# Optimization experiments

Measured on AMD Instinct MI355X. Metric: run time of the kernel, lower is better.

## Reference

```python
import jax, jax.numpy as jnp
import numpy as np
from jax import lax

N_GROUPS = 128
EPS = 1e-5


def _instance_norm(x):
    # x: [B, C, H, W]; per-sample per-channel normalization over spatial dims
    mean = jnp.mean(x, axis=(2, 3), keepdims=True)
    var = jnp.mean(jnp.square(x - mean), axis=(2, 3), keepdims=True)
    return (x - mean) * lax.rsqrt(var + EPS)


def _reflect_pad(x, p):
    return jnp.pad(x, ((0, 0), (0, 0), (p, p), (p, p)), mode='reflect')


def _conv(x, w, groups):
    # x: [N, Cin, H, W], w: [Cout, Cin/groups, kh, kw], VALID padding
    return lax.conv_general_dilated(
        x, w, window_strides=(1, 1), padding='VALID',
        dimension_numbers=('NCHW', 'OIHW', 'NCHW'),
        feature_group_count=groups)


def _forward_single(xi, ws, wp, b):
    # xi: [1, C, H, W]; ws: [C_mid, C/G, k, k]; wp: [C_pw, C_mid/G, 1, 1]; b: [C_pw]
    k = ws.shape[-1]
    p = (k - 1) // 2  # k=3 -> ceil/floor both 1
    y = _conv(_reflect_pad(xi, p), ws, N_GROUPS)
    y = _conv(y, wp, N_GROUPS) + b[None, :, None, None]
    return y


def setup_inputs() -> dict:
    key = jax.random.key(0)
    ks = jax.random.split(key, 6)
    B, C, H, W = 4, 512, 128, 128
    x = jax.random.normal(ks[0], (B, C, H, W), dtype=jnp.float32)
    w_spatial = jax.random.normal(ks[1], (B, 512, 4, 3, 3), dtype=jnp.float32) * 0.05
    w_pointwise = jax.random.normal(ks[2], (B, 128, 4, 1, 1), dtype=jnp.float32) * 0.05
    bias = jax.random.normal(ks[3], (B, 128), dtype=jnp.float32) * 0.05
    conv_w = jax.random.normal(ks[4], (512, 512, 3, 3), dtype=jnp.float32) * 0.02
    conv_b = jax.random.normal(ks[5], (512,), dtype=jnp.float32) * 0.02
    return {"x": x, "w_spatial": w_spatial, "w_pointwise": w_pointwise,
            "bias": bias, "conv_w": conv_w, "conv_b": conv_b}


def reference(x, w_spatial, w_pointwise, bias, conv_w, conv_b):
    B, C, H, W = x.shape
    x = _instance_norm(x)
    # per-sample grouped spatial + pointwise conv, vmapped over batch
    ys = jax.vmap(_forward_single)(x[:, None], w_spatial, w_pointwise, bias)
    # ys: [B, 1, C_pw, H, W] -> concat along channel dim as in torch.cat(dim=1)
    ys = ys.reshape(1, B * ys.shape[2], H, W)
    # final standard conv, reflect padding (1,1), kernel 3
    out = _conv(_reflect_pad(ys, 1), conv_w, 1) + conv_b[None, :, None, None]
    return out
```

## Files before the change

kernel.cpp:

```cpp
#include <hip/hip_runtime.h>
#include <hip/hip_bf16.h>


typedef unsigned short u16;
typedef __attribute__((ext_vector_type(8))) short bf16x8;
typedef __attribute__((ext_vector_type(4))) float f32x4;

#define HW 16384
#define NBC 2048

__device__ __forceinline__ int refl(int i) {
    return i < 0 ? -i : (i > 127 ? 254 - i : i);
}

__device__ __forceinline__ u16 f2bf(float f) {
    union { float f; unsigned u; } x; x.f = f;
    unsigned r = x.u + 0x7fffu + ((x.u >> 16) & 1u);
    return (u16)(r >> 16);
}

__device__ __forceinline__ void load_lds16(const u16* g, u16* l) {
    __builtin_amdgcn_global_load_lds(
        (const __attribute__((address_space(1))) unsigned int*)g,
        (__attribute__((address_space(3))) unsigned int*)l, 16, 0, 0);
}

__device__ __forceinline__ void load_lds4(const float* g, float* l) {
    __builtin_amdgcn_global_load_lds(
        (const __attribute__((address_space(1))) unsigned int*)g,
        (__attribute__((address_space(3))) unsigned int*)l, 4, 0, 0);
}

__global__ __launch_bounds__(256) void stats_kernel(
        const float* __restrict__ x, float* __restrict__ mean,
        float* __restrict__ rstd) {
    int bc = blockIdx.x;
    const float4* p4 = (const float4*)(x + (size_t)bc * HW);
    float s = 0.f, ss = 0.f;
    for (int i = threadIdx.x; i < HW / 4; i += 256) {
        float4 v = p4[i];
        s  += v.x + v.y + v.z + v.w;
        ss += v.x * v.x + v.y * v.y + v.z * v.z + v.w * v.w;
    }
    for (int o = 32; o >= 1; o >>= 1) {
        s  += __shfl_down(s, o);
        ss += __shfl_down(ss, o);
    }
    __shared__ float sm[4], sm2[4];
    int wid = threadIdx.x >> 6, lane = threadIdx.x & 63;
    if (lane == 0) { sm[wid] = s; sm2[wid] = ss; }
    __syncthreads();
    if (threadIdx.x == 0) {
        float S = sm[0] + sm[1] + sm[2] + sm[3];
        float SS = sm2[0] + sm2[1] + sm2[2] + sm2[3];
        float m = S * (1.f / HW);
        float var = SS * (1.f / HW) - m * m;
        mean[bc] = m;
        rstd[bc] = rsqrtf(var + 1e-5f);
    }
}

__global__ __launch_bounds__(256) void weff_kernel(
        const float* __restrict__ wsp, const float* __restrict__ wpw,
        float* __restrict__ we) {
    int idx = blockIdx.x * 256 + threadIdx.x;
    if (idx >= 4 * 128 * 4 * 9) return;
    int k = idx % 9;
    int c = (idx / 9) & 3;
    int g = (idx / 36) & 127;
    int b = idx / 4608;
    float acc = 0.f;
#pragma unroll
    for (int m = 0; m < 4; ++m) {
        acc += wpw[(b * 128 + g) * 4 + m] *
               wsp[(((size_t)b * 512 + g * 4 + m) * 4 + c) * 9 + k];
    }
    we[idx] = acc;
}

__global__ __launch_bounds__(256) void wpack_kernel(
        const float* __restrict__ cw, u16* __restrict__ wT) {
    __shared__ float s[512 * 10];
    int t = threadIdx.x, co = blockIdx.x;
    const float* src = cw + (size_t)co * 4608;
    for (int i = t; i < 4608; i += 256) {
        int ci = i / 9, tap = i - ci * 9;
        s[ci * 10 + tap] = src[i];
    }
    __syncthreads();
#pragma unroll
    for (int tap = 0; tap < 9; ++tap) {
        unsigned lo = (unsigned)f2bf(s[(2 * t) * 10 + tap]);
        unsigned hi = (unsigned)f2bf(s[(2 * t + 1) * 10 + tap]);
        ((unsigned*)&wT[((size_t)(tap << 9) + co) * 512])[t] = lo | (hi << 16);
    }
}

__global__ __launch_bounds__(512) void midconv_fused(
        const float* __restrict__ x, const float* __restrict__ mean,
        const float* __restrict__ rstd, const float* __restrict__ we,
        const float* __restrict__ bias, u16* __restrict__ ysT) {
    __shared__ float tile[16 * 324];
    __shared__ u16 outb[256 * 72];
    __shared__ float s_mean[512], s_rstd[512];
    __shared__ float s_w[144];
    __shared__ float s_bias[4];
    int t = threadIdx.x;
    int b = blockIdx.y;
    int x0 = (blockIdx.x & 7) << 4, y0 = (blockIdx.x >> 3) << 4;

    s_mean[t] = mean[(b << 9) + t];
    s_rstd[t] = rstd[(b << 9) + t];

    int soff[11];
#pragma unroll
    for (int s = 0; s < 11; ++s) {
        int idx = t + (s << 9);
        int id2 = idx < 5184 ? idx : 0;
        int c8 = id2 / 324;
        int rm = id2 - c8 * 324;
        int r = rm / 18, col = rm - r * 18;
        soff[s] = (c8 << 14) + (refl(y0 + r - 1) << 7) + refl(x0 + col - 1);
    }

    int gq = t >> 7;
    int rem = t & 127;
    int py = rem >> 3;
    int px0 = (rem & 7) << 1;
    const float* wq = &s_w[gq * 36];

    for (int q_i = 0; q_i < 32; ++q_i) {
        __syncthreads();
        if (q_i == 16) {
            for (int i = t; i < 2048; i += 512) {
                int pix = i >> 3, seg = i & 7;
                bf16x8 v = *(const bf16x8*)&outb[pix * 72 + (seg << 3)];
                int ppy = pix >> 4, ppx = pix & 15;
                size_t gp = (size_t)(((y0 + ppy) << 7) + x0 + ppx);
                *(bf16x8*)&ysT[gp * 512 + (b << 7) + (seg << 3)] = v;
            }
        }
        const float* xq = x + ((size_t)((b << 9) + (q_i << 4)) << 14);
#pragma unroll
        for (int s = 0; s < 10; ++s)
            load_lds4(xq + soff[s], &tile[t + (s << 9)]);
        if (t < 64) load_lds4(xq + soff[10], &tile[t + 5120]);
        if (t < 144) {
            int g_rel = t / 36, rr = t - g_rel * 36;
            int c = rr / 9;
            int group = (q_i << 2) + g_rel;
            s_w[t] = we[((b << 7) + group) * 36 + rr] *
                     s_rstd[(group << 2) + c];
        }
        if (t < 4) {
            int group = (q_i << 2) + t;
            float bsum = bias[(b << 7) + group];
            const float* wrow = we + ((b << 7) + group) * 36;
#pragma unroll
            for (int j = 0; j < 36; ++j) {
                int ch_l = (group << 2) + (j / 9);
                bsum -= wrow[j] * s_rstd[ch_l] * s_mean[ch_l];
            }
            s_bias[t] = bsum;
        }
        __syncthreads();
        float a0 = s_bias[gq], a1 = a0;
#pragma unroll
        for (int c = 0; c < 4; ++c) {
            const float* tp = &tile[(gq * 4 + c) * 324];
#pragma unroll
            for (int kh = 0; kh < 3; ++kh) {
                float2 u = *(const float2*)&tp[(py + kh) * 18 + px0];
                float2 v = *(const float2*)&tp[(py + kh) * 18 + px0 + 2];
                float w0 = wq[c * 9 + kh * 3 + 0];
                float w1 = wq[c * 9 + kh * 3 + 1];
                float w2 = wq[c * 9 + kh * 3 + 2];
                a0 += w0 * u.x + w1 * u.y + w2 * v.x;
                a1 += w0 * u.y + w1 * v.x + w2 * v.y;
            }
        }
        int col = ((q_i << 2) + gq) & 63;
        int pix = (py << 4) + px0;
        outb[pix * 72 + col] = f2bf(a0);
        outb[(pix + 1) * 72 + col] = f2bf(a1);
    }
    __syncthreads();
    for (int i = t; i < 2048; i += 512) {
        int pix = i >> 3, seg = i & 7;
        bf16x8 v = *(const bf16x8*)&outb[pix * 72 + (seg << 3)];
        int ppy = pix >> 4, ppx = pix & 15;
        size_t gp = (size_t)(((y0 + ppy) << 7) + x0 + ppx);
        *(bf16x8*)&ysT[gp * 512 + (b << 7) + 64 + (seg << 3)] = v;
    }
}

__global__ __launch_bounds__(256, 2) void finalconv_mfma(
        const u16* __restrict__ ysT, const u16* __restrict__ wT,
        const float* __restrict__ cb, float* __restrict__ out) {
    __shared__ u16 lds_ys[528 * 32];
    __shared__ u16 lds_wt[576 * 32];
    int t = threadIdx.x;
    int w = t >> 6, l = t & 63;
    int m = l & 15, q = l >> 4;
    int bid = blockIdx.x;
    int swz = ((bid & 7) << 6) + (bid >> 3);
    int co0 = (swz & 7) << 6;
    int y0 = (swz >> 3) << 1;
    int tr = w >> 1, xw = (w & 1) * 64;

    f32x4 acc[4][4];
#pragma unroll
    for (int i = 0; i < 4; ++i)
#pragma unroll
        for (int j = 0; j < 4; ++j) acc[i][j] = (f32x4){0.f, 0.f, 0.f, 0.f};

    for (int ci0 = 0; ci0 < 512; ci0 += 32) {
        __syncthreads();
        for (int i = w; i < 69; i += 4) {
            if (i < 33) {
                int s = i * 64 + l;
                int p = s >> 2, c = s & 3;
                int pc = p > 519 ? 519 : p;
                int hr = (pc * 1009) >> 17;
                int hc = pc - hr * 130;
                int gy = refl(y0 + hr - 1), gx = refl(hc - 1);
                int ci8 = c ^ ((p >> 1) & 3);
                const u16* src = ysT + (size_t)((gy << 7) + gx) * 512 + ci0 + ci8 * 8;
                load_lds16(src, &lds_ys[i * 512]);
            } else {
                int k = i - 33;
                int s = k * 64 + l;
                int row = s >> 2, c = s & 3;
                int tap = row >> 6, co_l = row & 63;
                int ci8 = c ^ ((co_l >> 1) & 3);
                const u16* src = wT + (size_t)((tap << 9) + co0 + co_l) * 512 + ci0 + ci8 * 8;
                load_lds16(src, &lds_wt[k * 512]);
            }
        }
        __syncthreads();
#pragma unroll
        for (int tap = 0; tap < 9; ++tap) {
            const int dyi = tap / 3, dxi = tap % 3;
            bf16x8 a[4], b[4];
#pragma unroll
            for (int i = 0; i < 4; ++i) {
                int co_l = i * 16 + m;
                int ch = q ^ ((co_l >> 1) & 3);
                a[i] = *(const bf16x8*)&lds_wt[(tap * 64 + co_l) * 32 + ch * 8];
            }
#pragma unroll
            for (int j = 0; j < 4; ++j) {
                int xx = xw + j * 16 + m;
                int p = (tr + dyi) * 130 + xx + dxi;
                int ch = q ^ ((p >> 1) & 3);
                b[j] = *(const bf16x8*)&lds_ys[p * 32 + ch * 8];
            }
#pragma unroll
            for (int i = 0; i < 4; ++i)
#pragma unroll
                for (int j = 0; j < 4; ++j)
                    acc[i][j] = __builtin_amdgcn_mfma_f32_16x16x32_bf16(
                        a[i], b[j], acc[i][j], 0, 0, 0);
        }
    }
    int gyo = y0 + tr;
#pragma unroll
    for (int i = 0; i < 4; ++i) {
        int cob = co0 + i * 16 + q * 4;
#pragma unroll
        for (int j = 0; j < 4; ++j) {
            int xx = xw + j * 16 + m;
            float* o = out + (size_t)cob * HW + (gyo << 7) + xx;
#pragma unroll
            for (int r = 0; r < 4; ++r)
                o[(size_t)r * HW] = acc[i][j][r] + cb[cob + r];
        }
    }
}

extern "C" void kernel_launch(void* const* d_in, const int* in_sizes, int n_in,
                              void* d_out, int out_size, void* d_ws, size_t ws_size,
                              hipStream_t stream) {
    const float* x    = (const float*)d_in[0];
    const float* wsp  = (const float*)d_in[1];
    const float* wpw  = (const float*)d_in[2];
    const float* bias = (const float*)d_in[3];
    const float* cw   = (const float*)d_in[4];
    const float* cb   = (const float*)d_in[5];
    float* out = (float*)d_out;

    char* ws = (char*)d_ws;
    u16*   ysT  = (u16*)ws;
    u16*   wT   = (u16*)(ws + 16777216);
    float* mean = (float*)(ws + 21495808);
    float* rstd = (float*)(ws + 21504000);
    float* we   = (float*)(ws + 21512192);

    stats_kernel<<<NBC, 256, 0, stream>>>(x, mean, rstd);
    weff_kernel<<<(4 * 128 * 4 * 9 + 255) / 256, 256, 0, stream>>>(wsp, wpw, we);
    wpack_kernel<<<512, 256, 0, stream>>>(cw, wT);
    midconv_fused<<<dim3(64, 4), 512, 0, stream>>>(x, mean, rstd, we, bias, ysT);
    finalconv_mfma<<<512, 256, 0, stream>>>(ysT, wT, cb, out);
}
```

Before: 372.8 us.

## Double-buffer midconv input tiles, shrink tile to 16x8, precompute folded weights

The grouped-conv kernel now uses 16x8 pixel tiles, giving twice as many blocks. It double-buffers the per-iteration channel slab in LDS with 16-byte async loads plus a separate halo buffer, so the next group's loads overlap the current compute. The rstd scaling and mean-derived bias are folded once into separate small kernels instead of being recomputed inside every block iteration. Each thread now computes one pixel instead of two, and wpack is simplified. The change adds an extra tiny launch and branchy halo reads in the inner loop.

```diff
diff --git a/kernel.cpp b/kernel.cpp
--- a/kernel.cpp
+++ b/kernel.cpp
@@ -20,6 +20,12 @@
 }
 
 __device__ __forceinline__ void load_lds16(const u16* g, u16* l) {
+    __builtin_amdgcn_global_load_lds(
+        (const __attribute__((address_space(1))) unsigned int*)g,
+        (__attribute__((address_space(3))) unsigned int*)l, 16, 0, 0);
+}
+
+__device__ __forceinline__ void load_lds16f(const float* g, float* l) {
     __builtin_amdgcn_global_load_lds(
         (const __attribute__((address_space(1))) unsigned int*)g,
         (__attribute__((address_space(3))) unsigned int*)l, 16, 0, 0);
@@ -62,7 +68,7 @@
 
 __global__ __launch_bounds__(256) void weff_kernel(
         const float* __restrict__ wsp, const float* __restrict__ wpw,
-        float* __restrict__ we) {
+        const float* __restrict__ rstd, float* __restrict__ wf) {
     int idx = blockIdx.x * 256 + threadIdx.x;
     if (idx >= 4 * 128 * 4 * 9) return;
     int k = idx % 9;
@@ -75,117 +81,122 @@
         acc += wpw[(b * 128 + g) * 4 + m] *
                wsp[(((size_t)b * 512 + g * 4 + m) * 4 + c) * 9 + k];
     }
-    we[idx] = acc;
+    wf[idx] = acc * rstd[(b << 9) + (g << 2) + c];
+}
+
+__global__ __launch_bounds__(256) void bias_fold(
+        const float* __restrict__ wf, const float* __restrict__ bias,
+        const float* __restrict__ mean, float* __restrict__ bf) {
+    int bg = blockIdx.x * 256 + threadIdx.x;
+    if (bg >= 512) return;
+    float s = bias[bg];
+    const float* w = wf + bg * 36;
+    const float* m = mean + (bg << 2);
+#pragma unroll
+    for (int j = 0; j < 36; ++j) s -= w[j] * m[j / 9];
+    bf[bg] = s;
 }
 
 __global__ __launch_bounds__(256) void wpack_kernel(
         const float* __restrict__ cw, u16* __restrict__ wT) {
-    __shared__ float s[512 * 10];
+    __shared__ float s[4608];
     int t = threadIdx.x, co = blockIdx.x;
     const float* src = cw + (size_t)co * 4608;
-    for (int i = t; i < 4608; i += 256) {
-        int ci = i / 9, tap = i - ci * 9;
-        s[ci * 10 + tap] = src[i];
-    }
+    for (int i = t; i < 4608; i += 256) s[i] = src[i];
     __syncthreads();
 #pragma unroll
     for (int tap = 0; tap < 9; ++tap) {
-        unsigned lo = (unsigned)f2bf(s[(2 * t) * 10 + tap]);
-        unsigned hi = (unsigned)f2bf(s[(2 * t + 1) * 10 + tap]);
-        ((unsigned*)&wT[((size_t)(tap << 9) + co) * 512])[t] = lo | (hi << 16);
+        u16* dst = &wT[((size_t)(tap << 9) + co) * 512];
+        dst[t]       = f2bf(s[t * 9 + tap]);
+        dst[t + 256] = f2bf(s[(t + 256) * 9 + tap]);
     }
 }
 
 __global__ __launch_bounds__(512) void midconv_fused(
-        const float* __restrict__ x, const float* __restrict__ mean,
-        const float* __restrict__ rstd, const float* __restrict__ we,
-        const float* __restrict__ bias, u16* __restrict__ ysT) {
-    __shared__ float tile[16 * 324];
-    __shared__ u16 outb[256 * 72];
-    __shared__ float s_mean[512], s_rstd[512];
-    __shared__ float s_w[144];
-    __shared__ float s_bias[4];
+        const float* __restrict__ x, const float* __restrict__ wf,
+        const float* __restrict__ bf, u16* __restrict__ ysT) {
+    __shared__ float mid[2][2560];
+    __shared__ float halo[2][320];
+    __shared__ u16 outb[128 * 72];
+    __shared__ float s_w[4608];
+    __shared__ float s_b[128];
     int t = threadIdx.x;
     int b = blockIdx.y;
-    int x0 = (blockIdx.x & 7) << 4, y0 = (blockIdx.x >> 3) << 4;
-
-    s_mean[t] = mean[(b << 9) + t];
-    s_rstd[t] = rstd[(b << 9) + t];
-
-    int soff[11];
-#pragma unroll
-    for (int s = 0; s < 11; ++s) {
-        int idx = t + (s << 9);
-        int id2 = idx < 5184 ? idx : 0;
-        int c8 = id2 / 324;
-        int rm = id2 - c8 * 324;
-        int r = rm / 18, col = rm - r * 18;
-        soff[s] = (c8 << 14) + (refl(y0 + r - 1) << 7) + refl(x0 + col - 1);
+    int x0 = (blockIdx.x & 7) << 4, y0 = (blockIdx.x >> 3) << 3;
+
+    for (int i = t; i < 4608; i += 512) s_w[i] = wf[b * 4608 + i];
+    if (t < 128) s_b[t] = bf[(b << 7) + t];
+
+    int smid0, smid1, shalo;
+    {
+        int ch = t / 40, rem = t - ch * 40;
+        int r = rem >> 2, j = rem & 3;
+        smid0 = (ch << 14) + (refl(y0 + r - 1) << 7) + x0 + (j << 2);
+        int i1 = t + 512 < 640 ? t + 512 : 0;
+        ch = i1 / 40; rem = i1 - ch * 40; r = rem >> 2; j = rem & 3;
+        smid1 = (ch << 14) + (refl(y0 + r - 1) << 7) + x0 + (j << 2);
+        int ih = t < 320 ? t : 0;
+        int side = ih >= 160;
+        int hh = side ? ih - 160 : ih;
+        ch = hh / 10; r = hh - ch * 10;
+        int col = side ? refl(x0 + 16) : refl(x0 - 1);
+        shalo = (ch << 14) + (refl(y0 + r - 1) << 7) + col;
     }
 
     int gq = t >> 7;
     int rem = t & 127;
-    int py = rem >> 3;
-    int px0 = (rem & 7) << 1;
-    const float* wq = &s_w[gq * 36];
-
-    for (int q_i = 0; q_i < 32; ++q_i) {
+    int py = rem >> 4, px = rem & 15;
+
+    {
+        const float* xq = x + ((size_t)(b << 9) << 14);
+        load_lds16f(xq + smid0, &mid[0][t * 4]);
+        if (t < 128) load_lds16f(xq + smid1, &mid[0][(512 + t) * 4]);
+        if (t < 320) load_lds4(xq + shalo, &halo[0][t]);
+    }
+
+    for (int q = 0; q < 32; ++q) {
         __syncthreads();
-        if (q_i == 16) {
-            for (int i = t; i < 2048; i += 512) {
+        if (q == 16) {
+            for (int i = t; i < 1024; i += 512) {
                 int pix = i >> 3, seg = i & 7;
                 bf16x8 v = *(const bf16x8*)&outb[pix * 72 + (seg << 3)];
                 int ppy = pix >> 4, ppx = pix & 15;
                 size_t gp = (size_t)(((y0 + ppy) << 7) + x0 + ppx);
                 *(bf16x8*)&ysT[gp * 512 + (b << 7) + (seg << 3)] = v;
             }
-        }
-        const float* xq = x + ((size_t)((b << 9) + (q_i << 4)) << 14);
-#pragma unroll
-        for (int s = 0; s < 10; ++s)
-            load_lds4(xq + soff[s], &tile[t + (s << 9)]);
-        if (t < 64) load_lds4(xq + soff[10], &tile[t + 5120]);
-        if (t < 144) {
-            int g_rel = t / 36, rr = t - g_rel * 36;
-            int c = rr / 9;
-            int group = (q_i << 2) + g_rel;
-            s_w[t] = we[((b << 7) + group) * 36 + rr] *
-                     s_rstd[(group << 2) + c];
-        }
-        if (t < 4) {
-            int group = (q_i << 2) + t;
-            float bsum = bias[(b << 7) + group];
-            const float* wrow = we + ((b << 7) + group) * 36;
-#pragma unroll
-            for (int j = 0; j < 36; ++j) {
-                int ch_l = (group << 2) + (j / 9);
-                bsum -= wrow[j] * s_rstd[ch_l] * s_mean[ch_l];
-            }
-            s_bias[t] = bsum;
-        }
-        __syncthreads();
-        float a0 = s_bias[gq], a1 = a0;
+            __syncthreads();
+        }
+        int cur = q & 1;
+        if (q < 31) {
+            const float* xq = x + ((size_t)((b << 9) + ((q + 1) << 4)) << 14);
+            load_lds16f(xq + smid0, &mid[cur ^ 1][t * 4]);
+            if (t < 128) load_lds16f(xq + smid1, &mid[cur ^ 1][(512 + t) * 4]);
+            if (t < 320) load_lds4(xq + shalo, &halo[cur ^ 1][t]);
+        }
+        int group = (q << 2) + gq;
+        float acc = s_b[group];
+        const float* wq = &s_w[group * 36];
 #pragma unroll
         for (int c = 0; c < 4; ++c) {
-            const float* tp = &tile[(gq * 4 + c) * 324];
+            const float* tp  = &mid[cur][(gq * 4 + c) * 160];
+            const float* hlc = &halo[cur][(gq * 4 + c) * 10];
+            const float* hrc = &halo[cur][160 + (gq * 4 + c) * 10];
 #pragma unroll
             for (int kh = 0; kh < 3; ++kh) {
-                float2 u = *(const float2*)&tp[(py + kh) * 18 + px0];
-                float2 v = *(const float2*)&tp[(py + kh) * 18 + px0 + 2];
-                float w0 = wq[c * 9 + kh * 3 + 0];
-                float w1 = wq[c * 9 + kh * 3 + 1];
-                float w2 = wq[c * 9 + kh * 3 + 2];
-                a0 += w0 * u.x + w1 * u.y + w2 * v.x;
-                a1 += w0 * u.y + w1 * v.x + w2 * v.y;
-            }
-        }
-        int col = ((q_i << 2) + gq) & 63;
-        int pix = (py << 4) + px0;
-        outb[pix * 72 + col] = f2bf(a0);
-        outb[(pix + 1) * 72 + col] = f2bf(a1);
+                int row = py + kh;
+                const float* rp = tp + row * 16;
+                float m0 = (px == 0)  ? hlc[row] : rp[px - 1];
+                float m1 = rp[px];
+                float m2 = (px == 15) ? hrc[row] : rp[px + 1];
+                acc += wq[c * 9 + kh * 3 + 0] * m0 +
+                       wq[c * 9 + kh * 3 + 1] * m1 +
+                       wq[c * 9 + kh * 3 + 2] * m2;
+            }
+        }
+        outb[(py * 16 + px) * 72 + (group & 63)] = f2bf(acc);
     }
     __syncthreads();
-    for (int i = t; i < 2048; i += 512) {
+    for (int i = t; i < 1024; i += 512) {
         int pix = i >> 3, seg = i & 7;
         bf16x8 v = *(const bf16x8*)&outb[pix * 72 + (seg << 3)];
         int ppy = pix >> 4, ppx = pix & 15;
@@ -294,11 +305,13 @@
     u16*   wT   = (u16*)(ws + 16777216);
     float* mean = (float*)(ws + 21495808);
     float* rstd = (float*)(ws + 21504000);
-    float* we   = (float*)(ws + 21512192);
+    float* wf   = (float*)(ws + 21512192);
+    float* bf   = (float*)(ws + 21585920);
 
     stats_kernel<<<NBC, 256, 0, stream>>>(x, mean, rstd);
-    weff_kernel<<<(4 * 128 * 4 * 9 + 255) / 256, 256, 0, stream>>>(wsp, wpw, we);
+    weff_kernel<<<(4 * 128 * 4 * 9 + 255) / 256, 256, 0, stream>>>(wsp, wpw, rstd, wf);
+    bias_fold<<<2, 256, 0, stream>>>(wf, bias, mean, bf);
     wpack_kernel<<<512, 256, 0, stream>>>(cw, wT);
-    midconv_fused<<<dim3(64, 4), 512, 0, stream>>>(x, mean, rstd, we, bias, ysT);
+    midconv_fused<<<dim3(128, 4), 512, 0, stream>>>(x, wf, bf, ysT);
     finalconv_mfma<<<512, 256, 0, stream>>>(ysT, wT, cb, out);
 }
```

After: 366.4 us. No clear change (-1.7%).
